# Kernel tuning notes

Measured on AMD Instinct MI355X. Metric: run time of the kernel, lower is better.

The kernel has to match this reference:

```python
import jax, jax.numpy as jnp
import numpy as np

VOCAB = 517015      # from nn.Embedding(517015, 300)
EMB_DIM = 300       # word_emb_dim
TOTAL_WORDS = 500_000
NUM_SENTS = 25_000  # avg 20 words per sentence


def setup_inputs() -> dict:
    key = jax.random.key(0)
    k_emb, k_ids = jax.random.split(key)
    word_emb = jax.random.normal(k_emb, (VOCAB, EMB_DIM), dtype=jnp.float32) * 0.1
    word_ids = jax.random.randint(k_ids, (TOTAL_WORDS,), 0, VOCAB, dtype=jnp.int32)
    # sorted segment ids, every segment nonempty (len(sent) >= 1 in real data)
    words_per_sent = TOTAL_WORDS // NUM_SENTS
    segment_ids = jnp.arange(TOTAL_WORDS, dtype=jnp.int32) // words_per_sent
    return {
        "word_emb": word_emb,
        "word_ids": word_ids,
        "segment_ids": segment_ids,
        "num_segments": NUM_SENTS,
    }


def reference(word_emb, word_ids, segment_ids, num_segments):
    # Packed equivalent of the nested Python loops:
    # per-word embedding gather, then per-sentence mean pooling
    # (np.sum(sent, axis=0) / len(sent) in the original).
    emb = word_emb[word_ids]                                      # [T, D]
    sums = jax.ops.segment_sum(emb, segment_ids,
                               num_segments=num_segments)         # [S, D]
    counts = jax.ops.segment_sum(
        jnp.ones((word_ids.shape[0], 1), dtype=emb.dtype),
        segment_ids, num_segments=num_segments)                   # [S, 1]
    return sums / counts                                          # [S, D]
```

## Files before the change

kernel.cpp:

```cpp
#include <hip/hip_runtime.h>

#define EMB_DIM 300
#define ROW_F4  75

__device__ __forceinline__ int lower_bound_i32(const int* __restrict__ a, int n, int key) {
    int lo = 0, hi = n;
    while (lo < hi) {
        int mid = (lo + hi) >> 1;
        if (a[mid] < key) lo = mid + 1; else hi = mid;
    }
    return lo;
}

__global__ __launch_bounds__(256) void emb_seg_mean_kernel(
        const float* __restrict__ emb,
        const int*   __restrict__ word_ids,
        const int*   __restrict__ seg_ids,
        float*       __restrict__ out,
        int num_segments, int total_words) {
    const int lane = threadIdx.x & 63;
    const int wave = threadIdx.x >> 6;
    const int s    = blockIdx.x * 4 + wave;
    if (s >= num_segments) return;

    const int start = lower_bound_i32(seg_ids, total_words, s);
    const int end   = lower_bound_i32(seg_ids, total_words, s + 1);
    const int count = end - start;

    int my_id = 0;
    if (start + lane < end) my_id = word_ids[start + lane];

    float4 acc0 = make_float4(0.f, 0.f, 0.f, 0.f);
    float4 acc1 = make_float4(0.f, 0.f, 0.f, 0.f);

    const int nb = count < 64 ? count : 64;
    for (int j = 0; j < nb; ++j) {
        const int id = __shfl(my_id, j);
        const float4* __restrict__ row = (const float4*)(emb + (size_t)id * EMB_DIM);
        float4 r0 = row[lane];
        acc0.x += r0.x; acc0.y += r0.y; acc0.z += r0.z; acc0.w += r0.w;
        if (lane < ROW_F4 - 64) {
            float4 r1 = row[64 + lane];
            acc1.x += r1.x; acc1.y += r1.y; acc1.z += r1.z; acc1.w += r1.w;
        }
    }
    for (int w = start + 64; w < end; ++w) {
        const int id = word_ids[w];
        const float4* __restrict__ row = (const float4*)(emb + (size_t)id * EMB_DIM);
        float4 r0 = row[lane];
        acc0.x += r0.x; acc0.y += r0.y; acc0.z += r0.z; acc0.w += r0.w;
        if (lane < ROW_F4 - 64) {
            float4 r1 = row[64 + lane];
            acc1.x += r1.x; acc1.y += r1.y; acc1.z += r1.z; acc1.w += r1.w;
        }
    }

    const float inv = 1.0f / (float)count;
    float4* __restrict__ orow = (float4*)(out + (size_t)s * EMB_DIM);
    orow[lane] = make_float4(acc0.x * inv, acc0.y * inv, acc0.z * inv, acc0.w * inv);
    if (lane < ROW_F4 - 64)
        orow[64 + lane] = make_float4(acc1.x * inv, acc1.y * inv, acc1.z * inv, acc1.w * inv);
}

extern "C" void kernel_launch(void* const* d_in, const int* in_sizes, int n_in,
                              void* d_out, int out_size, void* d_ws, size_t ws_size,
                              hipStream_t stream) {
    const float* emb      = (const float*)d_in[0];
    const int*   word_ids = (const int*)d_in[1];
    const int*   seg_ids  = (const int*)d_in[2];
    float* out = (float*)d_out;

    const int total_words  = in_sizes[1];
    const int num_segments = out_size / EMB_DIM;
    const int blocks = (num_segments + 3) / 4;

    emb_seg_mean_kernel<<<blocks, 256, 0, stream>>>(
        emb, word_ids, seg_ids, out, num_segments, total_words);
}
```

Before: 803.9 us.

## Precompute segment offsets in a boundary kernel and unroll gather loop by four

Replaces the two per-wave binary searches over segment ids with a separate pre-pass kernel that writes segment start offsets into the workspace by detecting boundaries. The main kernel reads start and end directly from that array. The gather loop is also unrolled by four so four row loads are in flight at once, which raises memory-level parallelism. The cost is an extra kernel launch plus workspace use, and it assumes every segment is nonempty, since empty segments would leave their start entries unset.

```diff
diff --git a/kernel.cpp b/kernel.cpp
--- a/kernel.cpp
+++ b/kernel.cpp
@@ -2,64 +2,92 @@
 
 #define EMB_DIM 300
 #define ROW_F4  75
+#define TAIL_F4 (ROW_F4 - 64)
 
-__device__ __forceinline__ int lower_bound_i32(const int* __restrict__ a, int n, int key) {
-    int lo = 0, hi = n;
-    while (lo < hi) {
-        int mid = (lo + hi) >> 1;
-        if (a[mid] < key) lo = mid + 1; else hi = mid;
+__global__ __launch_bounds__(256) void seg_starts_kernel(
+        const int* __restrict__ seg, int T, int S, int* __restrict__ starts) {
+    int t = blockIdx.x * 256 + threadIdx.x;
+    if (t >= T) return;
+    if (t == 0) {
+        starts[0] = 0;
+        starts[S] = T;
+    } else if (seg[t] != seg[t - 1]) {
+        starts[seg[t]] = t;
     }
-    return lo;
 }
 
 __global__ __launch_bounds__(256) void emb_seg_mean_kernel(
         const float* __restrict__ emb,
         const int*   __restrict__ word_ids,
-        const int*   __restrict__ seg_ids,
+        const int*   __restrict__ starts,
         float*       __restrict__ out,
-        int num_segments, int total_words) {
+        int num_segments) {
     const int lane = threadIdx.x & 63;
-    const int wave = threadIdx.x >> 6;
-    const int s    = blockIdx.x * 4 + wave;
+    const int s    = blockIdx.x * 4 + (threadIdx.x >> 6);
     if (s >= num_segments) return;
 
-    const int start = lower_bound_i32(seg_ids, total_words, s);
-    const int end   = lower_bound_i32(seg_ids, total_words, s + 1);
+    const int start = starts[s];
+    const int end   = starts[s + 1];
     const int count = end - start;
 
     int my_id = 0;
     if (start + lane < end) my_id = word_ids[start + lane];
 
-    float4 acc0 = make_float4(0.f, 0.f, 0.f, 0.f);
-    float4 acc1 = make_float4(0.f, 0.f, 0.f, 0.f);
+    float4 acc  = make_float4(0.f, 0.f, 0.f, 0.f);
+    float4 accT = make_float4(0.f, 0.f, 0.f, 0.f);
+    const bool tl = lane < TAIL_F4;
 
     const int nb = count < 64 ? count : 64;
-    for (int j = 0; j < nb; ++j) {
+    int j = 0;
+    for (; j + 4 <= nb; j += 4) {
+        const int i0 = __shfl(my_id, j);
+        const int i1 = __shfl(my_id, j + 1);
+        const int i2 = __shfl(my_id, j + 2);
+        const int i3 = __shfl(my_id, j + 3);
+        const float4* __restrict__ r0 = (const float4*)(emb + (size_t)i0 * EMB_DIM);
+        const float4* __restrict__ r1 = (const float4*)(emb + (size_t)i1 * EMB_DIM);
+        const float4* __restrict__ r2 = (const float4*)(emb + (size_t)i2 * EMB_DIM);
+        const float4* __restrict__ r3 = (const float4*)(emb + (size_t)i3 * EMB_DIM);
+        float4 a = r0[lane], b = r1[lane], c = r2[lane], d = r3[lane];
+        float4 at, bt, ct, dt;
+        if (tl) { at = r0[64 + lane]; bt = r1[64 + lane]; ct = r2[64 + lane]; dt = r3[64 + lane]; }
+        acc.x += (a.x + b.x) + (c.x + d.x);
+        acc.y += (a.y + b.y) + (c.y + d.y);
+        acc.z += (a.z + b.z) + (c.z + d.z);
+        acc.w += (a.w + b.w) + (c.w + d.w);
+        if (tl) {
+            accT.x += (at.x + bt.x) + (ct.x + dt.x);
+            accT.y += (at.y + bt.y) + (ct.y + dt.y);
+            accT.z += (at.z + bt.z) + (ct.z + dt.z);
+            accT.w += (at.w + bt.w) + (ct.w + dt.w);
+        }
+    }
+    for (; j < nb; ++j) {
         const int id = __shfl(my_id, j);
-        const float4* __restrict__ row = (const float4*)(emb + (size_t)id * EMB_DIM);
-        float4 r0 = row[lane];
-        acc0.x += r0.x; acc0.y += r0.y; acc0.z += r0.z; acc0.w += r0.w;
-        if (lane < ROW_F4 - 64) {
-            float4 r1 = row[64 + lane];
-            acc1.x += r1.x; acc1.y += r1.y; acc1.z += r1.z; acc1.w += r1.w;
+        const float4* __restrict__ r = (const float4*)(emb + (size_t)id * EMB_DIM);
+        float4 a = r[lane];
+        acc.x += a.x; acc.y += a.y; acc.z += a.z; acc.w += a.w;
+        if (tl) {
+            float4 at = r[64 + lane];
+            accT.x += at.x; accT.y += at.y; accT.z += at.z; accT.w += at.w;
         }
     }
     for (int w = start + 64; w < end; ++w) {
         const int id = word_ids[w];
-        const float4* __restrict__ row = (const float4*)(emb + (size_t)id * EMB_DIM);
-        float4 r0 = row[lane];
-        acc0.x += r0.x; acc0.y += r0.y; acc0.z += r0.z; acc0.w += r0.w;
-        if (lane < ROW_F4 - 64) {
-            float4 r1 = row[64 + lane];
-            acc1.x += r1.x; acc1.y += r1.y; acc1.z += r1.z; acc1.w += r1.w;
+        const float4* __restrict__ r = (const float4*)(emb + (size_t)id * EMB_DIM);
+        float4 a = r[lane];
+        acc.x += a.x; acc.y += a.y; acc.z += a.z; acc.w += a.w;
+        if (tl) {
+            float4 at = r[64 + lane];
+            accT.x += at.x; accT.y += at.y; accT.z += at.z; accT.w += at.w;
         }
     }
 
     const float inv = 1.0f / (float)count;
     float4* __restrict__ orow = (float4*)(out + (size_t)s * EMB_DIM);
-    orow[lane] = make_float4(acc0.x * inv, acc0.y * inv, acc0.z * inv, acc0.w * inv);
-    if (lane < ROW_F4 - 64)
-        orow[64 + lane] = make_float4(acc1.x * inv, acc1.y * inv, acc1.z * inv, acc1.w * inv);
+    orow[lane] = make_float4(acc.x * inv, acc.y * inv, acc.z * inv, acc.w * inv);
+    if (tl)
+        orow[64 + lane] = make_float4(accT.x * inv, accT.y * inv, accT.z * inv, accT.w * inv);
 }
 
 extern "C" void kernel_launch(void* const* d_in, const int* in_sizes, int n_in,
@@ -69,11 +97,13 @@
     const int*   word_ids = (const int*)d_in[1];
     const int*   seg_ids  = (const int*)d_in[2];
     float* out = (float*)d_out;
+    int* starts = (int*)d_ws;
 
-    const int total_words  = in_sizes[1];
-    const int num_segments = out_size / EMB_DIM;
-    const int blocks = (num_segments + 3) / 4;
+    const int T = in_sizes[1];
+    const int S = out_size / EMB_DIM;
 
-    emb_seg_mean_kernel<<<blocks, 256, 0, stream>>>(
-        emb, word_ids, seg_ids, out, num_segments, total_words);
+    seg_starts_kernel<<<(T + 255) / 256, 256, 0, stream>>>(seg_ids, T, S, starts);
+
+    const int blocks = (S + 3) / 4;
+    emb_seg_mean_kernel<<<blocks, 256, 0, stream>>>(emb, word_ids, starts, out, S);
 }
```

Result: faster. 770.1 us (-4.2%).
